# Kernel tuning notes

Hardware: AMD Instinct MI355X
Metric: run time of the kernel (lower is better)

The kernel has to match this reference:

```python
import jax, jax.numpy as jnp
import numpy as np

B, T, IN, H = 64, 1024, 512, 512

def setup_inputs() -> dict:
    key = jax.random.key(0)
    k1, k2, k3, k4, k5 = jax.random.split(key, 5)
    s_w = 1.0 / np.sqrt(IN)
    s_u = 1.0 / np.sqrt(H)
    return {
        "X": jax.random.normal(k1, (B, T, IN), dtype=jnp.float32),
        "h_0": jnp.zeros((B, H), dtype=jnp.float32),
        "W_w": jax.random.uniform(k2, (H, IN), jnp.float32, -s_w, s_w),
        "W_b": jax.random.uniform(k3, (H,), jnp.float32, -s_w, s_w),
        "U_w": jax.random.uniform(k4, (H, H), jnp.float32, -s_u, s_u),
        "U_b": jax.random.uniform(k5, (H,), jnp.float32, -s_u, s_u),
    }

def reference(X, h_0, W_w, W_b, U_w, U_b):
    # Precompute input projection for all timesteps: [B,T,H]
    Wx = jnp.einsum('bti,hi->bth', X, W_w) + W_b
    Wx_t = jnp.swapaxes(Wx, 0, 1)  # [T,B,H] for scan

    def step(h_prev, wx_t):
        h_t = jnp.tanh(wx_t + h_prev @ U_w.T + U_b)
        return h_t, h_t

    _, H_seq = jax.lax.scan(step, h_0, Wx_t)  # [T,B,H]
    return jnp.swapaxes(H_seq, 0, 1)  # [B,T,H]
```

## Files before the change

### kernel.cpp

```cpp
#include <hip/hip_runtime.h>
#include <cstdint>
#include <cstddef>


#define T_STEPS 1024

using f16 = _Float16;
typedef f16  f16x2 __attribute__((ext_vector_type(2)));
typedef f16  f16x8 __attribute__((ext_vector_type(8)));
typedef float f32x4 __attribute__((ext_vector_type(4)));

#if __has_builtin(__builtin_amdgcn_fdot2)
#define FDOT2(a, b, c) __builtin_amdgcn_fdot2((a), (b), (c), false)
#else
static __device__ __forceinline__ float FDOT2(f16x2 a, f16x2 b, float c) {
    return c + (float)a[0] * (float)b[0] + (float)a[1] * (float)b[1];
}
#endif

__global__ __launch_bounds__(256, 2)
void gemm_wx(const float* __restrict__ X, const float* __restrict__ W,
             const float* __restrict__ Wb, float* __restrict__ out) {
    __shared__ __align__(16) char Al[128 * 128];
    __shared__ __align__(16) char Bl[128 * 128];

    const int tid  = threadIdx.x;
    const int lane = tid & 63;
    const int wid  = tid >> 6;
    const int wm   = wid & 1;
    const int wn   = wid >> 1;
    const int m0   = blockIdx.x * 128;
    const int n0   = blockIdx.y * 128;

    f32x4 acc[4][4] = {};

    for (int kt = 0; kt < 512; kt += 64) {
        __syncthreads();
#pragma unroll
        for (int i = 0; i < 4; ++i) {
            const int id   = tid + i * 256;
            const int row  = id >> 3;
            const int slot = id & 7;
            const float4* pa = reinterpret_cast<const float4*>(
                X + (size_t)(m0 + row) * 512 + kt + slot * 8);
            const float4* pb = reinterpret_cast<const float4*>(
                W + (size_t)(n0 + row) * 512 + kt + slot * 8);
            float4 a0 = pa[0], a1 = pa[1];
            float4 b0 = pb[0], b1 = pb[1];
            f16x8 va = { (f16)a0.x, (f16)a0.y, (f16)a0.z, (f16)a0.w,
                         (f16)a1.x, (f16)a1.y, (f16)a1.z, (f16)a1.w };
            f16x8 vb = { (f16)b0.x, (f16)b0.y, (f16)b0.z, (f16)b0.w,
                         (f16)b1.x, (f16)b1.y, (f16)b1.z, (f16)b1.w };
            const int cb = (slot * 16) ^ ((row & 7) << 4);
            *reinterpret_cast<f16x8*>(Al + row * 128 + cb) = va;
            *reinterpret_cast<f16x8*>(Bl + row * 128 + cb) = vb;
        }
        __syncthreads();

#pragma unroll
        for (int kk = 0; kk < 2; ++kk) {
            f16x8 af[4], bf[4];
#pragma unroll
            for (int mi = 0; mi < 4; ++mi) {
                const int r  = wm * 64 + mi * 16 + (lane & 15);
                const int cb = (kk * 64 + ((lane >> 4) * 16)) ^ ((r & 7) << 4);
                af[mi] = *reinterpret_cast<const f16x8*>(Al + r * 128 + cb);
            }
#pragma unroll
            for (int ni = 0; ni < 4; ++ni) {
                const int r  = wn * 64 + ni * 16 + (lane & 15);
                const int cb = (kk * 64 + ((lane >> 4) * 16)) ^ ((r & 7) << 4);
                bf[ni] = *reinterpret_cast<const f16x8*>(Bl + r * 128 + cb);
            }
#pragma unroll
            for (int mi = 0; mi < 4; ++mi)
#pragma unroll
                for (int ni = 0; ni < 4; ++ni)
                    acc[mi][ni] = __builtin_amdgcn_mfma_f32_16x16x32_f16(
                        af[mi], bf[ni], acc[mi][ni], 0, 0, 0);
        }
    }

#pragma unroll
    for (int ni = 0; ni < 4; ++ni) {
        const int col  = n0 + wn * 64 + ni * 16 + (lane & 15);
        const float bias = Wb[col];
#pragma unroll
        for (int mi = 0; mi < 4; ++mi) {
            const int rowb = m0 + wm * 64 + mi * 16 + ((lane >> 4) * 4);
#pragma unroll
            for (int e = 0; e < 4; ++e)
                out[(size_t)(rowb + e) * 512 + col] = acc[mi][ni][e] + bias;
        }
    }
}

__global__ __launch_bounds__(1024)
void rnn_scan(float* __restrict__ out, const float* __restrict__ h0,
              const float* __restrict__ Uw, const float* __restrict__ Ub) {
    const int tid = threadIdx.x;
    const int b   = blockIdx.x;
    const int j   = tid >> 1;
    const int kh  = tid & 1;

    f16x2 u[128];
    {
        const float2* up = reinterpret_cast<const float2*>(
            Uw + (size_t)j * 512 + kh * 256);
#pragma unroll
        for (int r = 0; r < 128; ++r) {
            float2 v = up[r];
            u[r] = (f16x2){ (f16)v.x, (f16)v.y };
        }
    }
    const float ub = Ub[j];

    __shared__ __align__(16) char hbuf[2][1040];

    float* const obase = out + (size_t)b * (T_STEPS * 512);

    if (tid < 256) {
        const float2 v = reinterpret_cast<const float2*>(h0 + b * 512)[tid];
        f16x2 p = { (f16)v.x, (f16)v.y };
        *reinterpret_cast<unsigned*>(hbuf[0] + 4 * tid + (tid >= 128 ? 16 : 0)) =
            __builtin_bit_cast(unsigned, p);
    }
    float wx = (kh == 0) ? obase[j] : 0.0f;
    __syncthreads();

    for (int t = 0; t < T_STEPS; ++t) {
        float wxn = 0.0f;
        if (kh == 0 && t < T_STEPS - 1)
            wxn = obase[(size_t)(t + 1) * 512 + j];

        const uint4* hp = reinterpret_cast<const uint4*>(hbuf[t & 1] + kh * 528);
        float a0 = 0.f, a1 = 0.f, a2 = 0.f, a3 = 0.f;
#pragma unroll
        for (int r = 0; r < 32; ++r) {
            const uint4 hv = hp[r];
            a0 = FDOT2(u[4 * r + 0], __builtin_bit_cast(f16x2, hv.x), a0);
            a1 = FDOT2(u[4 * r + 1], __builtin_bit_cast(f16x2, hv.y), a1);
            a2 = FDOT2(u[4 * r + 2], __builtin_bit_cast(f16x2, hv.z), a2);
            a3 = FDOT2(u[4 * r + 3], __builtin_bit_cast(f16x2, hv.w), a3);
        }
        float acc = (a0 + a1) + (a2 + a3);
        acc += __shfl_xor(acc, 1);

        if (kh == 0) {
            const float a  = wx + acc + ub;
            const float ax = fabsf(a);
            const float e  = __expf(2.0f * ax);
            const float r1 = 1.0f - 2.0f / (e + 1.0f);
            const float h  = copysignf(r1, a);
            *reinterpret_cast<f16*>(hbuf[(t + 1) & 1] + 2 * j + (j >= 256 ? 16 : 0)) = (f16)h;
            obase[(size_t)t * 512 + j] = h;
        }
        wx = wxn;
        __syncthreads();
    }
}

extern "C" void kernel_launch(void* const* d_in, const int* in_sizes, int n_in,
                              void* d_out, int out_size, void* d_ws, size_t ws_size,
                              hipStream_t stream) {
    const float* X  = (const float*)d_in[0];
    const float* h0 = (const float*)d_in[1];
    const float* Ww = (const float*)d_in[2];
    const float* Wb = (const float*)d_in[3];
    const float* Uw = (const float*)d_in[4];
    const float* Ub = (const float*)d_in[5];
    float* out = (float*)d_out;

    gemm_wx<<<dim3(512, 4), dim3(256), 0, stream>>>(X, Ww, Wb, out);

    rnn_scan<<<dim3(64), dim3(1024), 0, stream>>>(out, h0, Uw, Ub);
}
```

Baseline: 2.860 ms.

## Give each scan thread a full U row, broadcasting h via readlane

After: 2.335 ms. -18.4%, faster.

```diff
diff --git a/kernel.cpp b/kernel.cpp
--- a/kernel.cpp
+++ b/kernel.cpp
@@ -17,6 +17,10 @@
     return c + (float)a[0] * (float)b[0] + (float)a[1] * (float)b[1];
 }
 #endif
+
+static __device__ __forceinline__ f16x2 bcast_pair(int v) {
+    return __builtin_bit_cast(f16x2, v);
+}
 
 __global__ __launch_bounds__(256, 2)
 void gemm_wx(const float* __restrict__ X, const float* __restrict__ W,
@@ -95,66 +99,88 @@
     }
 }
 
-__global__ __launch_bounds__(1024)
+#define KREG   448
+#define NPREG  (KREG / 2)
+
+__global__ __launch_bounds__(512, 2)
 void rnn_scan(float* __restrict__ out, const float* __restrict__ h0,
               const float* __restrict__ Uw, const float* __restrict__ Ub) {
-    const int tid = threadIdx.x;
-    const int b   = blockIdx.x;
-    const int j   = tid >> 1;
-    const int kh  = tid & 1;
-
-    f16x2 u[128];
+    const int tid  = threadIdx.x;
+    const int b    = blockIdx.x;
+    const int lane = tid & 63;
+
+    f16x2 u[NPREG];
     {
-        const float2* up = reinterpret_cast<const float2*>(
-            Uw + (size_t)j * 512 + kh * 256);
-#pragma unroll
-        for (int r = 0; r < 128; ++r) {
-            float2 v = up[r];
-            u[r] = (f16x2){ (f16)v.x, (f16)v.y };
-        }
-    }
-    const float ub = Ub[j];
-
-    __shared__ __align__(16) char hbuf[2][1040];
+        const float2* up = reinterpret_cast<const float2*>(Uw + (size_t)tid * 512);
+#pragma unroll
+        for (int p = 0; p < NPREG; ++p) {
+            float2 v = up[p];
+            u[p] = (f16x2){ (f16)v.x, (f16)v.y };
+        }
+    }
+    const float ub = Ub[tid];
+
+    __shared__ __align__(16) char utail[512 * 128];
+    __shared__ __align__(16) char hb[2][1024];
+
+    {
+        const float4* tp = reinterpret_cast<const float4*>(Uw + (size_t)tid * 512 + KREG);
+#pragma unroll
+        for (int i = 0; i < 8; ++i) {
+            float4 v0 = tp[2 * i], v1 = tp[2 * i + 1];
+            f16x8 w = { (f16)v0.x, (f16)v0.y, (f16)v0.z, (f16)v0.w,
+                        (f16)v1.x, (f16)v1.y, (f16)v1.z, (f16)v1.w };
+            *reinterpret_cast<f16x8*>(utail + tid * 128 + ((16 * i) ^ ((tid & 7) << 4))) = w;
+        }
+    }
 
     float* const obase = out + (size_t)b * (T_STEPS * 512);
 
-    if (tid < 256) {
-        const float2 v = reinterpret_cast<const float2*>(h0 + b * 512)[tid];
-        f16x2 p = { (f16)v.x, (f16)v.y };
-        *reinterpret_cast<unsigned*>(hbuf[0] + 4 * tid + (tid >= 128 ? 16 : 0)) =
-            __builtin_bit_cast(unsigned, p);
-    }
-    float wx = (kh == 0) ? obase[j] : 0.0f;
+    *reinterpret_cast<f16*>(hb[0] + 2 * tid) = (f16)h0[b * 512 + tid];
+    float wx = obase[tid];
     __syncthreads();
 
     for (int t = 0; t < T_STEPS; ++t) {
+        const uint4 vh = *reinterpret_cast<const uint4*>(hb[t & 1] + 16 * lane);
         float wxn = 0.0f;
-        if (kh == 0 && t < T_STEPS - 1)
-            wxn = obase[(size_t)(t + 1) * 512 + j];
-
-        const uint4* hp = reinterpret_cast<const uint4*>(hbuf[t & 1] + kh * 528);
+        if (t < T_STEPS - 1) wxn = obase[(size_t)(t + 1) * 512 + tid];
+
         float a0 = 0.f, a1 = 0.f, a2 = 0.f, a3 = 0.f;
 #pragma unroll
-        for (int r = 0; r < 32; ++r) {
-            const uint4 hv = hp[r];
-            a0 = FDOT2(u[4 * r + 0], __builtin_bit_cast(f16x2, hv.x), a0);
-            a1 = FDOT2(u[4 * r + 1], __builtin_bit_cast(f16x2, hv.y), a1);
-            a2 = FDOT2(u[4 * r + 2], __builtin_bit_cast(f16x2, hv.z), a2);
-            a3 = FDOT2(u[4 * r + 3], __builtin_bit_cast(f16x2, hv.w), a3);
-        }
-        float acc = (a0 + a1) + (a2 + a3);
-        acc += __shfl_xor(acc, 1);
-
-        if (kh == 0) {
-            const float a  = wx + acc + ub;
-            const float ax = fabsf(a);
-            const float e  = __expf(2.0f * ax);
-            const float r1 = 1.0f - 2.0f / (e + 1.0f);
-            const float h  = copysignf(r1, a);
-            *reinterpret_cast<f16*>(hbuf[(t + 1) & 1] + 2 * j + (j >= 256 ? 16 : 0)) = (f16)h;
-            obase[(size_t)t * 512 + j] = h;
-        }
+        for (int p = 0; p < NPREG; p += 4) {
+            const int ln = p >> 2;
+            const int s0 = __builtin_amdgcn_readlane((int)vh.x, ln);
+            const int s1 = __builtin_amdgcn_readlane((int)vh.y, ln);
+            const int s2 = __builtin_amdgcn_readlane((int)vh.z, ln);
+            const int s3 = __builtin_amdgcn_readlane((int)vh.w, ln);
+            a0 = FDOT2(bcast_pair(s0), u[p + 0], a0);
+            a1 = FDOT2(bcast_pair(s1), u[p + 1], a1);
+            a2 = FDOT2(bcast_pair(s2), u[p + 2], a2);
+            a3 = FDOT2(bcast_pair(s3), u[p + 3], a3);
+        }
+#pragma unroll
+        for (int i = 0; i < 8; ++i) {
+            const uint4 ut = *reinterpret_cast<const uint4*>(
+                utail + tid * 128 + ((16 * i) ^ ((tid & 7) << 4)));
+            const int ln = 56 + i;
+            const int s0 = __builtin_amdgcn_readlane((int)vh.x, ln);
+            const int s1 = __builtin_amdgcn_readlane((int)vh.y, ln);
+            const int s2 = __builtin_amdgcn_readlane((int)vh.z, ln);
+            const int s3 = __builtin_amdgcn_readlane((int)vh.w, ln);
+            a0 = FDOT2(bcast_pair(s0), __builtin_bit_cast(f16x2, ut.x), a0);
+            a1 = FDOT2(bcast_pair(s1), __builtin_bit_cast(f16x2, ut.y), a1);
+            a2 = FDOT2(bcast_pair(s2), __builtin_bit_cast(f16x2, ut.z), a2);
+            a3 = FDOT2(bcast_pair(s3), __builtin_bit_cast(f16x2, ut.w), a3);
+        }
+
+        const float a  = wx + ((a0 + a1) + (a2 + a3)) + ub;
+        const float ax = fabsf(a);
+        const float e  = __expf(2.0f * ax);
+        const float r1 = 1.0f - 2.0f / (e + 1.0f);
+        const float h  = copysignf(r1, a);
+
+        *reinterpret_cast<f16*>(hb[(t + 1) & 1] + 2 * tid) = (f16)h;
+        obase[(size_t)t * 512 + tid] = h;
         wx = wxn;
         __syncthreads();
     }
@@ -172,6 +198,5 @@
     float* out = (float*)d_out;
 
     gemm_wx<<<dim3(512, 4), dim3(256), 0, stream>>>(X, Ww, Wb, out);
-
-    rnn_scan<<<dim3(64), dim3(1024), 0, stream>>>(out, h0, Uw, Ub);
-}
+    rnn_scan<<<dim3(64), dim3(512), 0, stream>>>(out, h0, Uw, Ub);
+}
```

## Batch 16 sequences per block and compute recurrent matvec with MFMA

Applied to the files above, without the earlier changes.

Result: slower. 4.932 ms (+72.4%).

```diff
diff --git a/kernel.cpp b/kernel.cpp
--- a/kernel.cpp
+++ b/kernel.cpp
@@ -10,17 +10,15 @@
 typedef f16  f16x8 __attribute__((ext_vector_type(8)));
 typedef float f32x4 __attribute__((ext_vector_type(4)));
 
-#if __has_builtin(__builtin_amdgcn_fdot2)
-#define FDOT2(a, b, c) __builtin_amdgcn_fdot2((a), (b), (c), false)
-#else
-static __device__ __forceinline__ float FDOT2(f16x2 a, f16x2 b, float c) {
-    return c + (float)a[0] * (float)b[0] + (float)a[1] * (float)b[1];
-}
-#endif
+static __device__ __forceinline__ f16x8 cvt8(float4 v0, float4 v1) {
+    return (f16x8){ (f16)v0.x, (f16)v0.y, (f16)v0.z, (f16)v0.w,
+                    (f16)v1.x, (f16)v1.y, (f16)v1.z, (f16)v1.w };
+}
 
 __global__ __launch_bounds__(256, 2)
 void gemm_wx(const float* __restrict__ X, const float* __restrict__ W,
-             const float* __restrict__ Wb, float* __restrict__ out) {
+             const float* __restrict__ Wb, const float* __restrict__ Ub,
+             float* __restrict__ out) {
     __shared__ __align__(16) char Al[128 * 128];
     __shared__ __align__(16) char Bl[128 * 128];
 
@@ -45,12 +43,8 @@
                 X + (size_t)(m0 + row) * 512 + kt + slot * 8);
             const float4* pb = reinterpret_cast<const float4*>(
                 W + (size_t)(n0 + row) * 512 + kt + slot * 8);
-            float4 a0 = pa[0], a1 = pa[1];
-            float4 b0 = pb[0], b1 = pb[1];
-            f16x8 va = { (f16)a0.x, (f16)a0.y, (f16)a0.z, (f16)a0.w,
-                         (f16)a1.x, (f16)a1.y, (f16)a1.z, (f16)a1.w };
-            f16x8 vb = { (f16)b0.x, (f16)b0.y, (f16)b0.z, (f16)b0.w,
-                         (f16)b1.x, (f16)b1.y, (f16)b1.z, (f16)b1.w };
+            f16x8 va = cvt8(pa[0], pa[1]);
+            f16x8 vb = cvt8(pb[0], pb[1]);
             const int cb = (slot * 16) ^ ((row & 7) << 4);
             *reinterpret_cast<f16x8*>(Al + row * 128 + cb) = va;
             *reinterpret_cast<f16x8*>(Bl + row * 128 + cb) = vb;
@@ -84,7 +78,7 @@
 #pragma unroll
     for (int ni = 0; ni < 4; ++ni) {
         const int col  = n0 + wn * 64 + ni * 16 + (lane & 15);
-        const float bias = Wb[col];
+        const float bias = Wb[col] + Ub[col];
 #pragma unroll
         for (int mi = 0; mi < 4; ++mi) {
             const int rowb = m0 + wm * 64 + mi * 16 + ((lane >> 4) * 4);
@@ -95,68 +89,134 @@
     }
 }
 
-__global__ __launch_bounds__(1024)
+__global__ __launch_bounds__(512, 2)
 void rnn_scan(float* __restrict__ out, const float* __restrict__ h0,
-              const float* __restrict__ Uw, const float* __restrict__ Ub) {
-    const int tid = threadIdx.x;
-    const int b   = blockIdx.x;
-    const int j   = tid >> 1;
-    const int kh  = tid & 1;
-
-    f16x2 u[128];
+              const float* __restrict__ Uw) {
+    __shared__ __align__(16) char Ul[512 * 256];
+    __shared__ __align__(16) char Hs[16 * 1024];
+
+    const int tid  = threadIdx.x;
+    const int wid  = tid >> 6;
+    const int lane = tid & 63;
+    const int l15  = lane & 15;
+    const int l4   = lane >> 4;
+    const int n0w  = wid * 64;
+    const int b0   = blockIdx.x * 16;
+    const int aswz = (l15 & 7) << 4;
+
     {
-        const float2* up = reinterpret_cast<const float2*>(
-            Uw + (size_t)j * 512 + kh * 256);
-#pragma unroll
-        for (int r = 0; r < 128; ++r) {
-            float2 v = up[r];
-            u[r] = (f16x2){ (f16)v.x, (f16)v.y };
-        }
-    }
-    const float ub = Ub[j];
-
-    __shared__ __align__(16) char hbuf[2][1040];
-
-    float* const obase = out + (size_t)b * (T_STEPS * 512);
-
-    if (tid < 256) {
-        const float2 v = reinterpret_cast<const float2*>(h0 + b * 512)[tid];
-        f16x2 p = { (f16)v.x, (f16)v.y };
-        *reinterpret_cast<unsigned*>(hbuf[0] + 4 * tid + (tid >= 128 ? 16 : 0)) =
-            __builtin_bit_cast(unsigned, p);
-    }
-    float wx = (kh == 0) ? obase[j] : 0.0f;
+        const float4* src = reinterpret_cast<const float4*>(Uw + (size_t)tid * 512 + 384);
+        const int sw = (tid & 7) << 4;
+#pragma unroll
+        for (int i = 0; i < 16; ++i) {
+            f16x8 w = cvt8(src[2 * i], src[2 * i + 1]);
+            *reinterpret_cast<f16x8*>(Ul + tid * 256 + ((16 * i) ^ sw)) = w;
+        }
+    }
+
+    f16x8 u[12][4];
+#pragma unroll
+    for (int kk = 0; kk < 12; ++kk)
+#pragma unroll
+        for (int nt = 0; nt < 4; ++nt) {
+            const float4* p = reinterpret_cast<const float4*>(
+                Uw + (size_t)(n0w + nt * 16 + l15) * 512 + kk * 32 + l4 * 8);
+            u[kk][nt] = cvt8(p[0], p[1]);
+        }
+
+    {
+        const int m = tid >> 5, c = tid & 31;
+        const float4* p = reinterpret_cast<const float4*>(
+            h0 + (size_t)(b0 + m) * 512 + c * 16);
+        f16x8 w0 = cvt8(p[0], p[1]);
+        f16x8 w1 = cvt8(p[2], p[3]);
+        const int mb = m * 1024, sw = (m & 7) << 4;
+        *reinterpret_cast<f16x8*>(Hs + mb + ((c * 32) ^ sw)) = w0;
+        *reinterpret_cast<f16x8*>(Hs + mb + ((c * 32 + 16) ^ sw)) = w1;
+    }
+
+    float* const outg = out + (size_t)b0 * (T_STEPS * 512);
+    int offe[4];
+#pragma unroll
+    for (int e = 0; e < 4; ++e)
+        offe[e] = ((l4 * 4 + e) * (T_STEPS * 512) + (n0w + l15)) * 4;
+
     __syncthreads();
 
     for (int t = 0; t < T_STEPS; ++t) {
-        float wxn = 0.0f;
-        if (kh == 0 && t < T_STEPS - 1)
-            wxn = obase[(size_t)(t + 1) * 512 + j];
-
-        const uint4* hp = reinterpret_cast<const uint4*>(hbuf[t & 1] + kh * 528);
-        float a0 = 0.f, a1 = 0.f, a2 = 0.f, a3 = 0.f;
-#pragma unroll
-        for (int r = 0; r < 32; ++r) {
-            const uint4 hv = hp[r];
-            a0 = FDOT2(u[4 * r + 0], __builtin_bit_cast(f16x2, hv.x), a0);
-            a1 = FDOT2(u[4 * r + 1], __builtin_bit_cast(f16x2, hv.y), a1);
-            a2 = FDOT2(u[4 * r + 2], __builtin_bit_cast(f16x2, hv.z), a2);
-            a3 = FDOT2(u[4 * r + 3], __builtin_bit_cast(f16x2, hv.w), a3);
-        }
-        float acc = (a0 + a1) + (a2 + a3);
-        acc += __shfl_xor(acc, 1);
-
-        if (kh == 0) {
-            const float a  = wx + acc + ub;
-            const float ax = fabsf(a);
-            const float e  = __expf(2.0f * ax);
-            const float r1 = 1.0f - 2.0f / (e + 1.0f);
-            const float h  = copysignf(r1, a);
-            *reinterpret_cast<f16*>(hbuf[(t + 1) & 1] + 2 * j + (j >= 256 ? 16 : 0)) = (f16)h;
-            obase[(size_t)t * 512 + j] = h;
-        }
-        wx = wxn;
-        __syncthreads();
+        float wx[4][4];
+#pragma unroll
+        for (int e = 0; e < 4; ++e) {
+            const float* pe = reinterpret_cast<const float*>(
+                reinterpret_cast<const char*>(outg) + offe[e]);
+#pragma unroll
+            for (int nt = 0; nt < 4; ++nt)
+                wx[nt][e] = pe[nt * 16];
+        }
+
+        f32x4 acc[4];
+#pragma unroll
+        for (int nt = 0; nt < 4; ++nt) acc[nt] = (f32x4){0.f, 0.f, 0.f, 0.f};
+#pragma unroll
+        for (int kk = 0; kk < 16; ++kk) {
+            const f16x8 a = *reinterpret_cast<const f16x8*>(
+                Hs + l15 * 1024 + ((kk * 64 + l4 * 16) ^ aswz));
+            if (kk < 12) {
+#pragma unroll
+                for (int nt = 0; nt < 4; ++nt)
+                    acc[nt] = __builtin_amdgcn_mfma_f32_16x16x32_f16(
+                        a, u[kk][nt], acc[nt], 0, 0, 0);
+            } else {
+#pragma unroll
+                for (int nt = 0; nt < 4; ++nt) {
+                    const f16x8 bb = *reinterpret_cast<const f16x8*>(
+                        Ul + (size_t)(n0w + nt * 16 + l15) * 256 +
+                        (((kk - 12) * 64 + l4 * 16) ^ aswz));
+                    acc[nt] = __builtin_amdgcn_mfma_f32_16x16x32_f16(
+                        a, bb, acc[nt], 0, 0, 0);
+                }
+            }
+        }
+
+        float hv[4][4];
+#pragma unroll
+        for (int nt = 0; nt < 4; ++nt)
+#pragma unroll
+            for (int e = 0; e < 4; ++e) {
+                const float aa = acc[nt][e] + wx[nt][e];
+                const float ax = fabsf(aa);
+                const float ex = __expf(2.0f * ax);
+                const float r1 = 1.0f - 2.0f / (ex + 1.0f);
+                hv[nt][e] = copysignf(r1, aa);
+            }
+#pragma unroll
+        for (int e = 0; e < 4; ++e) {
+            float* pe = reinterpret_cast<float*>(
+                reinterpret_cast<char*>(outg) + offe[e]);
+#pragma unroll
+            for (int nt = 0; nt < 4; ++nt)
+                pe[nt * 16] = hv[nt][e];
+            offe[e] += 2048;
+        }
+
+        __builtin_amdgcn_sched_barrier(0);
+        __builtin_amdgcn_s_barrier();
+        __builtin_amdgcn_sched_barrier(0);
+
+#pragma unroll
+        for (int nt = 0; nt < 4; ++nt) {
+            const int j2 = 2 * (n0w + nt * 16 + l15);
+#pragma unroll
+            for (int e = 0; e < 4; ++e) {
+                const int m = l4 * 4 + e;
+                *reinterpret_cast<f16*>(Hs + m * 1024 + (j2 ^ ((m & 7) << 4))) =
+                    (f16)hv[nt][e];
+            }
+        }
+
+        asm volatile("s_waitcnt lgkmcnt(0)" ::: "memory");
+        __builtin_amdgcn_s_barrier();
+        __builtin_amdgcn_sched_barrier(0);
     }
 }
 
@@ -171,7 +231,6 @@
     const float* Ub = (const float*)d_in[5];
     float* out = (float*)d_out;
 
-    gemm_wx<<<dim3(512, 4), dim3(256), 0, stream>>>(X, Ww, Wb, out);
-
-    rnn_scan<<<dim3(64), dim3(1024), 0, stream>>>(out, h0, Uw, Ub);
-}
+    gemm_wx<<<dim3(512, 4), dim3(256), 0, stream>>>(X, Ww, Wb, Ub, out);
+    rnn_scan<<<dim3(4), dim3(512), 0, stream>>>(out, h0, Uw);
+}
```
